# Performance work log

Hardware: AMD Instinct MI355X
Metric: run time of the kernel (lower is better)

The kernel has to match this reference:

```python
import jax, jax.numpy as jnp
import numpy as np


def setup_inputs() -> dict:
    key = jax.random.key(0)
    k1, k2 = jax.random.split(key)
    B, S, D, E = 8, 8192, 512, 209
    x = jax.random.normal(k1, (B, S, D), dtype=jnp.float32)
    # nn.init.normal_(std=0.01)
    gate_w = jax.random.normal(k2, (E, D), dtype=jnp.float32) * 0.01
    expert_counts = jnp.zeros((E,), dtype=jnp.float32)
    gate_probs_sum = jnp.zeros((E,), dtype=jnp.float32)
    return {"x": x, "gate_w": gate_w, "expert_counts": expert_counts,
            "gate_probs_sum": gate_probs_sum}


def reference(x, gate_w, expert_counts, gate_probs_sum):
    B, S, D = x.shape
    E = gate_w.shape[0]
    x_flat = x.reshape(-1, D)                      # [N, D]
    n_tokens = x_flat.shape[0]
    gate_logits = jnp.einsum('nd,ed->ne', x_flat, gate_w)   # [N, E]
    gate_probs = jax.nn.softmax(gate_logits, axis=-1)
    gate_scores = jnp.max(gate_probs, axis=-1)               # [N]
    expert_indices = jnp.argmax(gate_probs, axis=-1)         # [N] int
    # one-hot sum over tokens == histogram of expert assignments
    tokens_per_expert_actual = jnp.zeros((E,), dtype=jnp.float32).at[expert_indices].add(1.0)
    gate_mean = jnp.mean(gate_probs, axis=0)                 # [E]
    load_balancing_loss = E * jnp.sum(gate_mean * tokens_per_expert_actual) / n_tokens
    # EMA buffer updates (no-grad in the original)
    new_expert_counts = 0.9 * expert_counts + 0.1 * tokens_per_expert_actual
    new_gate_probs_sum = 0.9 * gate_probs_sum + 0.1 * jnp.sum(gate_probs, axis=0)
    return (x_flat, gate_scores, expert_indices, load_balancing_loss,
            new_expert_counts, new_gate_probs_sum)
```

## Files before the change

### kernel.cpp

```cpp
#include <hip/hip_runtime.h>

#define DK 512
#define TMB 128
#define KB 32
#define NCHUNK (DK / KB)
#define NPANEL 14
#define EPAD 224
#define LP 225
#define WFRAG_ELEMS (EPAD * DK)

typedef __attribute__((ext_vector_type(8))) short bf16x8;
typedef __attribute__((ext_vector_type(4))) float f32x4;

__device__ __forceinline__ unsigned short f2b(float f) {
    unsigned u = __float_as_uint(f);
    return (unsigned short)((u + 0x7fffu + ((u >> 16) & 1u)) >> 16);
}
__device__ __forceinline__ float b2f(unsigned short h) {
    return __uint_as_float((unsigned)h << 16);
}
__device__ __forceinline__ void split4(float4 v, ushort4& h, ushort4& lo) {
    h.x = f2b(v.x); h.y = f2b(v.y); h.z = f2b(v.z); h.w = f2b(v.w);
    lo.x = f2b(v.x - b2f(h.x)); lo.y = f2b(v.y - b2f(h.y));
    lo.z = f2b(v.z - b2f(h.z)); lo.w = f2b(v.w - b2f(h.w));
}
__device__ __forceinline__ void split4t(float4 v, ushort4& h, ushort4& lo) {
    unsigned ux = __float_as_uint(v.x), uy = __float_as_uint(v.y);
    unsigned uz = __float_as_uint(v.z), uw = __float_as_uint(v.w);
    h.x = (unsigned short)(ux >> 16); h.y = (unsigned short)(uy >> 16);
    h.z = (unsigned short)(uz >> 16); h.w = (unsigned short)(uw >> 16);
    lo.x = f2b(v.x - __uint_as_float(ux & 0xffff0000u));
    lo.y = f2b(v.y - __uint_as_float(uy & 0xffff0000u));
    lo.z = f2b(v.z - __uint_as_float(uz & 0xffff0000u));
    lo.w = f2b(v.w - __uint_as_float(uw & 0xffff0000u));
}
__device__ __forceinline__ int swz(int row, int colbyte) {
    return (row * 64 + colbyte) ^ ((row & 7) << 4);
}

extern "C" __global__ void moe_init(float* hist, float* probsum, int* cnt) {
    int t = threadIdx.x;
    if (t < EPAD) { hist[t] = 0.f; probsum[t] = 0.f; }
    if (t == 0) *cnt = 0;
}

extern "C" __global__ void __launch_bounds__(256)
moe_prep(const float* __restrict__ w,
         unsigned short* __restrict__ wHi,
         unsigned short* __restrict__ wLo, int E)
{
    int g = blockIdx.x * 256 + threadIdx.x;
    int l  = g & 63;
    int pc = g >> 6;
    int ch = pc / NPANEL;
    int p  = pc - ch * NPANEL;
    int e  = p * 16 + (l & 15);
    int k0 = ch * KB + (l >> 4) * 8;
    float4 v0 = make_float4(0.f,0.f,0.f,0.f), v1 = v0;
    if (e < E) {
        v0 = *(const float4*)(w + (size_t)e * DK + k0);
        v1 = *(const float4*)(w + (size_t)e * DK + k0 + 4);
    }
    ushort4 h0, l0, h1, l1;
    split4(v0, h0, l0); split4(v1, h1, l1);
    size_t off = (size_t)g * 8;
    *(ushort4*)(wHi + off)     = h0;
    *(ushort4*)(wHi + off + 4) = h1;
    *(ushort4*)(wLo + off)     = l0;
    *(ushort4*)(wLo + off + 4) = l1;
}

extern "C" __global__ void __launch_bounds__(256, 2)
moe_main(const float* __restrict__ x,
         const unsigned short* __restrict__ wHi,
         const unsigned short* __restrict__ wLo,
         float* __restrict__ out,
         float* __restrict__ hist,
         float* __restrict__ probsum_g,
         int* __restrict__ flag_cnt,
         int* __restrict__ flag_list,
         int flag_cap, int N, int E)
{
    __shared__ float logits_s[32 * LP];
    __shared__ float ps_l[EPAD];
    __shared__ float tok_m[32], tok_s[32];
    char* base = (char*)logits_s;
    char* Ahi = base;
    char* Alo = base + 8192;

    const int t    = threadIdx.x;
    const int l    = t & 63;
    const int wm   = t >> 6;
    const int lrow = l & 15;
    const int coff = (l >> 4) * 16;
    const int tok0 = blockIdx.x * TMB;

    f32x4 acc[2][NPANEL];
    #pragma unroll
    for (int mi = 0; mi < 2; ++mi)
        #pragma unroll
        for (int pp = 0; pp < NPANEL; ++pp)
            acc[mi][pp] = (f32x4){0.f, 0.f, 0.f, 0.f};

    for (int ch = 0; ch < NCHUNK; ++ch) {
        __syncthreads();
        #pragma unroll
        for (int i = 0; i < 4; ++i) {
            int u = t + 256 * i;
            int row = u >> 3, c4 = (u & 7) * 4;
            size_t g = (size_t)(tok0 + row) * DK + ch * KB + c4;
            float4 v = *(const float4*)(x + g);
            *(float4*)(out + g) = v;
            ushort4 h, lo; split4t(v, h, lo);
            int off = swz(row, c4 * 2);
            *(ushort4*)(Ahi + off) = h;
            *(ushort4*)(Alo + off) = lo;
        }
        __syncthreads();
        bf16x8 ah[2], al[2];
        #pragma unroll
        for (int mi = 0; mi < 2; ++mi) {
            int off = swz(wm * 32 + mi * 16 + lrow, coff);
            ah[mi] = *(const bf16x8*)(Ahi + off);
            al[mi] = *(const bf16x8*)(Alo + off);
        }
        #pragma unroll
        for (int pp = 0; pp < NPANEL; ++pp) {
            size_t boff = ((size_t)(ch * NPANEL + pp) * 64 + l) * 8;
            bf16x8 bh = *(const bf16x8*)(wHi + boff);
            bf16x8 bl = *(const bf16x8*)(wLo + boff);
            #pragma unroll
            for (int mi = 0; mi < 2; ++mi) {
                acc[mi][pp] = __builtin_amdgcn_mfma_f32_16x16x32_bf16(ah[mi], bh, acc[mi][pp], 0, 0, 0);
                acc[mi][pp] = __builtin_amdgcn_mfma_f32_16x16x32_bf16(ah[mi], bl, acc[mi][pp], 0, 0, 0);
                acc[mi][pp] = __builtin_amdgcn_mfma_f32_16x16x32_bf16(al[mi], bh, acc[mi][pp], 0, 0, 0);
            }
        }
    }

    if (t < EPAD) ps_l[t] = 0.f;
    float* logits = logits_s;

    for (int pass = 0; pass < 4; ++pass) {
        __syncthreads();
        if (wm == pass) {
            #pragma unroll
            for (int mi = 0; mi < 2; ++mi)
                #pragma unroll
                for (int pp = 0; pp < NPANEL; ++pp)
                    #pragma unroll
                    for (int rg = 0; rg < 4; ++rg) {
                        int rr = mi * 16 + (l >> 4) * 4 + rg;
                        int cc = pp * 16 + lrow;
                        logits[rr * LP + cc] = acc[mi][pp][rg];
                    }
        }
        __syncthreads();
        {
            int r = t >> 3, sub = t & 7;
            float m1 = -1e30f, m2 = -1e30f;
            int i1 = 0x7fffffff;
            for (int e = sub; e < E; e += 8) {
                float v = logits[r * LP + e];
                if (v > m1) { m2 = m1; m1 = v; i1 = e; }
                else if (v > m2) { m2 = v; }
            }
            #pragma unroll
            for (int mask = 1; mask < 8; mask <<= 1) {
                float om1 = __shfl_xor(m1, mask);
                float om2 = __shfl_xor(m2, mask);
                int   oi1 = __shfl_xor(i1, mask);
                if (om1 > m1 || (om1 == m1 && oi1 < i1)) {
                    m2 = fmaxf(m1, om2); m1 = om1; i1 = oi1;
                } else {
                    m2 = fmaxf(m2, om1);
                }
            }
            float s = 0.f;
            for (int e = sub; e < E; e += 8) s += __expf(logits[r * LP + e] - m1);
            #pragma unroll
            for (int mask = 1; mask < 8; mask <<= 1) s += __shfl_xor(s, mask);

            if (sub == 0) {
                float sinv = 1.0f / s;
                tok_m[r] = m1; tok_s[r] = sinv;
                int tok = tok0 + pass * 32 + r;
                out[(size_t)N * DK + tok]     = sinv;
                out[(size_t)N * DK + N + tok] = (float)i1;
                atomicAdd(&hist[i1], 1.0f);
                if (m1 - m2 < 1e-4f) {
                    int pos = atomicAdd(flag_cnt, 1);
                    if (pos < flag_cap) flag_list[pos] = tok;
                }
            }
        }
        __syncthreads();
        if (t < E) {
            float sum = 0.f;
            #pragma unroll 4
            for (int r = 0; r < 32; ++r)
                sum += __expf(logits[r * LP + t] - tok_m[r]) * tok_s[r];
            ps_l[t] += sum;
        }
    }
    __syncthreads();
    if (t < E) atomicAdd(&probsum_g[t], ps_l[t]);
}

extern "C" __global__ void __launch_bounds__(256)
moe_refine(const float* __restrict__ x,
           const float* __restrict__ w,
           float* __restrict__ hist,
           const int* __restrict__ flag_cnt,
           const int* __restrict__ flag_list,
           int flag_cap,
           float* __restrict__ out,
           int N, int E)
{
    __shared__ float  xsh[DK];
    __shared__ double rv[256];
    __shared__ int    ri[256];
    int nf = *flag_cnt; if (nf > flag_cap) nf = flag_cap;
    const int tid = threadIdx.x;

    for (int li = blockIdx.x; li < nf; li += gridDim.x) {
        int tok = flag_list[li];
        for (int k = tid; k < DK; k += 256) xsh[k] = x[(size_t)tok * DK + k];
        __syncthreads();
        double a = -1e300;
        if (tid < E) {
            const float* wr = w + (size_t)tid * DK;
            double a0 = 0, a1 = 0, a2 = 0, a3 = 0;
            for (int k = 0; k < DK; k += 4) {
                a0 += (double)xsh[k]     * (double)wr[k];
                a1 += (double)xsh[k + 1] * (double)wr[k + 1];
                a2 += (double)xsh[k + 2] * (double)wr[k + 2];
                a3 += (double)xsh[k + 3] * (double)wr[k + 3];
            }
            a = (a0 + a1) + (a2 + a3);
        }
        rv[tid] = a; ri[tid] = tid;
        __syncthreads();
        for (int s = 128; s > 0; s >>= 1) {
            if (tid < s) {
                double vb = rv[tid + s]; int ib = ri[tid + s];
                double va = rv[tid];     int ia = ri[tid];
                if (vb > va || (vb == va && ib < ia)) { rv[tid] = vb; ri[tid] = ib; }
            }
            __syncthreads();
        }
        if (tid == 0) {
            int newi = ri[0];
            int oldi = (int)out[(size_t)N * DK + N + tok];
            if (newi != oldi) {
                atomicAdd(&hist[oldi], -1.0f);
                atomicAdd(&hist[newi],  1.0f);
                out[(size_t)N * DK + N + tok] = (float)newi;
            }
        }
        __syncthreads();
    }
}

extern "C" __global__ void __launch_bounds__(256)
moe_final(const float* __restrict__ hist,
          const float* __restrict__ probsum,
          const float* __restrict__ ec_in,
          const float* __restrict__ gps_in,
          float* __restrict__ out,
          int N, int E)
{
    __shared__ double red[256];
    int t = threadIdx.x;
    double p = 0.0;
    if (t < E) p = (double)hist[t] * (double)probsum[t];
    red[t] = p;
    __syncthreads();
    for (int s = 128; s > 0; s >>= 1) {
        if (t < s) red[t] += red[t + s];
        __syncthreads();
    }
    size_t base = (size_t)N * DK + 2 * (size_t)N;
    if (t == 0) {
        double loss = (double)E * red[0] / ((double)N * (double)N);
        out[base] = (float)loss;
    }
    if (t < E) {
        out[base + 1 + t]     = 0.9f * ec_in[t]  + 0.1f * hist[t];
        out[base + 1 + E + t] = 0.9f * gps_in[t] + 0.1f * probsum[t];
    }
}

extern "C" void kernel_launch(void* const* d_in, const int* in_sizes, int n_in,
                              void* d_out, int out_size, void* d_ws, size_t ws_size,
                              hipStream_t stream)
{
    const float* x   = (const float*)d_in[0];
    const float* w   = (const float*)d_in[1];
    const float* ec  = (const float*)d_in[2];
    const float* gps = (const float*)d_in[3];
    float* out = (float*)d_out;

    int E = in_sizes[2];
    int N = in_sizes[0] / DK;

    unsigned short* wHi = (unsigned short*)d_ws;
    unsigned short* wLo = wHi + WFRAG_ELEMS;
    float* hist    = (float*)(wLo + WFRAG_ELEMS);
    float* probsum = hist + EPAD;
    int*   cnt     = (int*)(probsum + EPAD);
    int*   list    = cnt + 1;
    long long used = 2LL * WFRAG_ELEMS * 2 + 4LL * (2 * EPAD + 1);
    long long cap_ll = ((long long)ws_size - used) / 4;
    int cap = cap_ll < 0 ? 0 : (cap_ll > 65536 ? 65536 : (int)cap_ll);

    moe_prep  <<<56,      256, 0, stream>>>(w, wHi, wLo, E);
    moe_init  <<<1,       256, 0, stream>>>(hist, probsum, cnt);
    moe_main  <<<N / TMB, 256, 0, stream>>>(x, wHi, wLo, out, hist, probsum, cnt, list, cap, N, E);
    moe_refine<<<256,     256, 0, stream>>>(x, w, hist, cnt, list, cap, out, N, E);
    moe_final <<<1,       256, 0, stream>>>(hist, probsum, ec, gps, out, N, E);
}
```

Baseline: 218.3 us.

## Load A fragments directly to registers and do softmax epilogue in-register

Each wave now loads its own 32 token rows straight from global memory into MFMA fragment registers, splitting them into bf16 hi/lo parts. This removes the shared-memory A staging and its per-chunk barriers. The softmax, argmax and column prob-sum are computed directly on the accumulator registers using cross-lane shuffles, replacing the shared logits buffer and its four serialized passes. The cost is less coalesced global loads (each lane reads a 32-byte strided segment per row) and higher register pressure.

```diff
diff --git a/kernel.cpp b/kernel.cpp
--- a/kernel.cpp
+++ b/kernel.cpp
@@ -2,11 +2,9 @@
 
 #define DK 512
 #define TMB 128
-#define KB 32
-#define NCHUNK (DK / KB)
+#define NSTEP 16
 #define NPANEL 14
 #define EPAD 224
-#define LP 225
 #define WFRAG_ELEMS (EPAD * DK)
 
 typedef __attribute__((ext_vector_type(8))) short bf16x8;
@@ -24,18 +22,14 @@
     lo.x = f2b(v.x - b2f(h.x)); lo.y = f2b(v.y - b2f(h.y));
     lo.z = f2b(v.z - b2f(h.z)); lo.w = f2b(v.w - b2f(h.w));
 }
-__device__ __forceinline__ void split4t(float4 v, ushort4& h, ushort4& lo) {
-    unsigned ux = __float_as_uint(v.x), uy = __float_as_uint(v.y);
-    unsigned uz = __float_as_uint(v.z), uw = __float_as_uint(v.w);
-    h.x = (unsigned short)(ux >> 16); h.y = (unsigned short)(uy >> 16);
-    h.z = (unsigned short)(uz >> 16); h.w = (unsigned short)(uw >> 16);
-    lo.x = f2b(v.x - __uint_as_float(ux & 0xffff0000u));
-    lo.y = f2b(v.y - __uint_as_float(uy & 0xffff0000u));
-    lo.z = f2b(v.z - __uint_as_float(uz & 0xffff0000u));
-    lo.w = f2b(v.w - __uint_as_float(uw & 0xffff0000u));
-}
-__device__ __forceinline__ int swz(int row, int colbyte) {
-    return (row * 64 + colbyte) ^ ((row & 7) << 4);
+__device__ __forceinline__ void pack8(float4 a, float4 b, bf16x8& h, bf16x8& lo) {
+    float v[8] = {a.x, a.y, a.z, a.w, b.x, b.y, b.z, b.w};
+    #pragma unroll
+    for (int j = 0; j < 8; ++j) {
+        unsigned u = __float_as_uint(v[j]);
+        h[j]  = (short)(u >> 16);
+        lo[j] = (short)f2b(v[j] - __uint_as_float(u & 0xffff0000u));
+    }
 }
 
 extern "C" __global__ void moe_init(float* hist, float* probsum, int* cnt) {
@@ -52,10 +46,10 @@
     int g = blockIdx.x * 256 + threadIdx.x;
     int l  = g & 63;
     int pc = g >> 6;
-    int ch = pc / NPANEL;
-    int p  = pc - ch * NPANEL;
+    int kk = pc / NPANEL;
+    int p  = pc - kk * NPANEL;
     int e  = p * 16 + (l & 15);
-    int k0 = ch * KB + (l >> 4) * 8;
+    int k0 = kk * 32 + (l >> 4) * 8;
     float4 v0 = make_float4(0.f,0.f,0.f,0.f), v1 = v0;
     if (e < E) {
         v0 = *(const float4*)(w + (size_t)e * DK + k0);
@@ -81,19 +75,21 @@
          int* __restrict__ flag_list,
          int flag_cap, int N, int E)
 {
-    __shared__ float logits_s[32 * LP];
     __shared__ float ps_l[EPAD];
-    __shared__ float tok_m[32], tok_s[32];
-    char* base = (char*)logits_s;
-    char* Ahi = base;
-    char* Alo = base + 8192;
-
-    const int t    = threadIdx.x;
-    const int l    = t & 63;
-    const int wm   = t >> 6;
-    const int lrow = l & 15;
-    const int coff = (l >> 4) * 16;
-    const int tok0 = blockIdx.x * TMB;
+
+    const int t  = threadIdx.x;
+    const int l  = t & 63;
+    const int wm = t >> 6;
+    const int le = l & 15;
+    const int lg = l >> 4;
+    const int tok0 = blockIdx.x * TMB + wm * 32;
+
+    if (t < EPAD) ps_l[t] = 0.f;
+
+    const float* xr0 = x + (size_t)(tok0 + le) * DK + lg * 8;
+    const float* xr1 = xr0 + (size_t)16 * DK;
+    float* ow0 = out + (size_t)(tok0 + le) * DK + lg * 8;
+    float* ow1 = ow0 + (size_t)16 * DK;
 
     f32x4 acc[2][NPANEL];
     #pragma unroll
@@ -102,71 +98,49 @@
         for (int pp = 0; pp < NPANEL; ++pp)
             acc[mi][pp] = (f32x4){0.f, 0.f, 0.f, 0.f};
 
-    for (int ch = 0; ch < NCHUNK; ++ch) {
-        __syncthreads();
-        #pragma unroll
-        for (int i = 0; i < 4; ++i) {
-            int u = t + 256 * i;
-            int row = u >> 3, c4 = (u & 7) * 4;
-            size_t g = (size_t)(tok0 + row) * DK + ch * KB + c4;
-            float4 v = *(const float4*)(x + g);
-            *(float4*)(out + g) = v;
-            ushort4 h, lo; split4t(v, h, lo);
-            int off = swz(row, c4 * 2);
-            *(ushort4*)(Ahi + off) = h;
-            *(ushort4*)(Alo + off) = lo;
-        }
-        __syncthreads();
-        bf16x8 ah[2], al[2];
-        #pragma unroll
-        for (int mi = 0; mi < 2; ++mi) {
-            int off = swz(wm * 32 + mi * 16 + lrow, coff);
-            ah[mi] = *(const bf16x8*)(Ahi + off);
-            al[mi] = *(const bf16x8*)(Alo + off);
-        }
+    #pragma unroll 2
+    for (int kk = 0; kk < NSTEP; ++kk) {
+        float4 a00 = *(const float4*)(xr0 + kk * 32);
+        float4 a01 = *(const float4*)(xr0 + kk * 32 + 4);
+        float4 a10 = *(const float4*)(xr1 + kk * 32);
+        float4 a11 = *(const float4*)(xr1 + kk * 32 + 4);
+        *(float4*)(ow0 + kk * 32)     = a00;
+        *(float4*)(ow0 + kk * 32 + 4) = a01;
+        *(float4*)(ow1 + kk * 32)     = a10;
+        *(float4*)(ow1 + kk * 32 + 4) = a11;
+        bf16x8 ah0, al0, ah1, al1;
+        pack8(a00, a01, ah0, al0);
+        pack8(a10, a11, ah1, al1);
         #pragma unroll
         for (int pp = 0; pp < NPANEL; ++pp) {
-            size_t boff = ((size_t)(ch * NPANEL + pp) * 64 + l) * 8;
+            size_t boff = ((size_t)(kk * NPANEL + pp) * 64 + l) * 8;
             bf16x8 bh = *(const bf16x8*)(wHi + boff);
             bf16x8 bl = *(const bf16x8*)(wLo + boff);
-            #pragma unroll
-            for (int mi = 0; mi < 2; ++mi) {
-                acc[mi][pp] = __builtin_amdgcn_mfma_f32_16x16x32_bf16(ah[mi], bh, acc[mi][pp], 0, 0, 0);
-                acc[mi][pp] = __builtin_amdgcn_mfma_f32_16x16x32_bf16(ah[mi], bl, acc[mi][pp], 0, 0, 0);
-                acc[mi][pp] = __builtin_amdgcn_mfma_f32_16x16x32_bf16(al[mi], bh, acc[mi][pp], 0, 0, 0);
-            }
-        }
-    }
-
-    if (t < EPAD) ps_l[t] = 0.f;
-    float* logits = logits_s;
-
-    for (int pass = 0; pass < 4; ++pass) {
-        __syncthreads();
-        if (wm == pass) {
-            #pragma unroll
-            for (int mi = 0; mi < 2; ++mi)
-                #pragma unroll
-                for (int pp = 0; pp < NPANEL; ++pp)
-                    #pragma unroll
-                    for (int rg = 0; rg < 4; ++rg) {
-                        int rr = mi * 16 + (l >> 4) * 4 + rg;
-                        int cc = pp * 16 + lrow;
-                        logits[rr * LP + cc] = acc[mi][pp][rg];
-                    }
-        }
-        __syncthreads();
-        {
-            int r = t >> 3, sub = t & 7;
-            float m1 = -1e30f, m2 = -1e30f;
-            int i1 = 0x7fffffff;
-            for (int e = sub; e < E; e += 8) {
-                float v = logits[r * LP + e];
+            acc[0][pp] = __builtin_amdgcn_mfma_f32_16x16x32_bf16(ah0, bh, acc[0][pp], 0, 0, 0);
+            acc[0][pp] = __builtin_amdgcn_mfma_f32_16x16x32_bf16(ah0, bl, acc[0][pp], 0, 0, 0);
+            acc[0][pp] = __builtin_amdgcn_mfma_f32_16x16x32_bf16(al0, bh, acc[0][pp], 0, 0, 0);
+            acc[1][pp] = __builtin_amdgcn_mfma_f32_16x16x32_bf16(ah1, bh, acc[1][pp], 0, 0, 0);
+            acc[1][pp] = __builtin_amdgcn_mfma_f32_16x16x32_bf16(ah1, bl, acc[1][pp], 0, 0, 0);
+            acc[1][pp] = __builtin_amdgcn_mfma_f32_16x16x32_bf16(al1, bh, acc[1][pp], 0, 0, 0);
+        }
+    }
+
+    float m1r[8], svr[8];
+    #pragma unroll
+    for (int mi = 0; mi < 2; ++mi) {
+        #pragma unroll
+        for (int rg = 0; rg < 4; ++rg) {
+            const int r8 = mi * 4 + rg;
+            float m1 = -1e30f, m2 = -1e30f; int i1 = 0x7fff;
+            #pragma unroll
+            for (int pp = 0; pp < NPANEL; ++pp) {
+                int e = pp * 16 + le;
+                float v = (e < E) ? acc[mi][pp][rg] : -1e30f;
                 if (v > m1) { m2 = m1; m1 = v; i1 = e; }
                 else if (v > m2) { m2 = v; }
             }
             #pragma unroll
-            for (int mask = 1; mask < 8; mask <<= 1) {
+            for (int mask = 1; mask < 16; mask <<= 1) {
                 float om1 = __shfl_xor(m1, mask);
                 float om2 = __shfl_xor(m2, mask);
                 int   oi1 = __shfl_xor(i1, mask);
@@ -177,14 +151,18 @@
                 }
             }
             float s = 0.f;
-            for (int e = sub; e < E; e += 8) s += __expf(logits[r * LP + e] - m1);
-            #pragma unroll
-            for (int mask = 1; mask < 8; mask <<= 1) s += __shfl_xor(s, mask);
-
-            if (sub == 0) {
-                float sinv = 1.0f / s;
-                tok_m[r] = m1; tok_s[r] = sinv;
-                int tok = tok0 + pass * 32 + r;
+            #pragma unroll
+            for (int pp = 0; pp < NPANEL; ++pp) {
+                int e = pp * 16 + le;
+                float v = (e < E) ? acc[mi][pp][rg] : -1e30f;
+                s += __expf(v - m1);
+            }
+            #pragma unroll
+            for (int mask = 1; mask < 16; mask <<= 1) s += __shfl_xor(s, mask);
+            float sinv = 1.0f / s;
+            m1r[r8] = m1; svr[r8] = sinv;
+            if (le == 0) {
+                int tok = tok0 + mi * 16 + lg * 4 + rg;
                 out[(size_t)N * DK + tok]     = sinv;
                 out[(size_t)N * DK + N + tok] = (float)i1;
                 atomicAdd(&hist[i1], 1.0f);
@@ -194,13 +172,30 @@
                 }
             }
         }
-        __syncthreads();
-        if (t < E) {
-            float sum = 0.f;
-            #pragma unroll 4
-            for (int r = 0; r < 32; ++r)
-                sum += __expf(logits[r * LP + t] - tok_m[r]) * tok_s[r];
-            ps_l[t] += sum;
+    }
+
+    float ps[NPANEL];
+    #pragma unroll
+    for (int pp = 0; pp < NPANEL; ++pp) {
+        float sum = 0.f;
+        #pragma unroll
+        for (int mi = 0; mi < 2; ++mi)
+            #pragma unroll
+            for (int rg = 0; rg < 4; ++rg) {
+                int e = pp * 16 + le;
+                float v = (e < E) ? acc[mi][pp][rg] : -1e30f;
+                sum += __expf(v - m1r[mi * 4 + rg]) * svr[mi * 4 + rg];
+            }
+        sum += __shfl_xor(sum, 16);
+        sum += __shfl_xor(sum, 32);
+        ps[pp] = sum;
+    }
+    __syncthreads();
+    if (lg == 0) {
+        #pragma unroll
+        for (int pp = 0; pp < NPANEL; ++pp) {
+            int e = pp * 16 + le;
+            if (e < E) atomicAdd(&ps_l[e], ps[pp]);
         }
     }
     __syncthreads();
```

After: 243.7 us. +11.6%, slower.
